# Optimization experiments

Hardware: AMD Instinct MI355X
Metric: run time of the kernel (lower is better)

## Reference

```python
import jax, jax.numpy as jnp
import numpy as np

N = 8192
D_IN = 128
D_OUT = 128

def setup_inputs() -> dict:
    key = jax.random.key(0)
    k_x, k_q, k_k, k_v = jax.random.split(key, 4)
    scale = 1.0 / np.sqrt(D_IN)
    return {
        "input": jax.random.normal(k_x, (N, D_IN), dtype=jnp.float32),
        # torch Linear weights: [out_features, in_features]
        "Wq": jax.random.normal(k_q, (D_IN, D_IN), dtype=jnp.float32) * scale,
        "Wk": jax.random.normal(k_k, (D_IN, D_IN), dtype=jnp.float32) * scale,
        "Wv": jax.random.normal(k_v, (D_OUT, D_IN), dtype=jnp.float32) * scale,
    }

def reference(input, Wq, Wk, Wv):
    # torch Linear: y = x @ W.T
    Q = input @ Wq.T          # [N, d_in]
    K = input @ Wk.T          # [N, d_in]
    V = input @ Wv.T          # [N, d_out]
    # NOTE: original module has NO 1/sqrt(d) scaling — keep it faithful.
    W = jax.nn.softmax(Q @ K.T, axis=-1)  # [N, N]
    return W @ V              # [N, d_out]
```

## Files before the change

kernel.cpp:

```cpp
#include <hip/hip_runtime.h>
#include <hip/hip_bf16.h>
#include <stdint.h>

#define N_TOK 8192
#define D 128
#define QTILES (N_TOK / 16)
#define KVB 64
#define KVTILES (N_TOK / KVB)

typedef __attribute__((ext_vector_type(8))) short short8;
typedef __attribute__((ext_vector_type(4))) short short4v;
typedef __attribute__((ext_vector_type(4))) float f32x4;
typedef __attribute__((ext_vector_type(8))) _Float16 half8;
typedef __attribute__((ext_vector_type(4))) _Float16 half4;
typedef __attribute__((ext_vector_type(2))) __fp16 fp16x2;

__device__ __forceinline__ ushort f2bf(float f) {
    union { float f; uint32_t u; } cv; cv.f = f;
    uint32_t u = cv.u;
    return (ushort)((u + 0x7fffu + ((u >> 16) & 1u)) >> 16);
}
__device__ __forceinline__ float bf2f(ushort h) {
    union { uint32_t u; float f; } cv; cv.u = ((uint32_t)h) << 16;
    return cv.f;
}
__device__ __forceinline__ f32x4 zero4() {
    f32x4 z; z[0] = 0.f; z[1] = 0.f; z[2] = 0.f; z[3] = 0.f; return z;
}

__global__ void cvt_kernel(const float* __restrict__ Wq, const float* __restrict__ Wk,
                           const float* __restrict__ Wv,
                           ushort* __restrict__ Whi, ushort* __restrict__ Wlo) {
    int i = blockIdx.x * blockDim.x + threadIdx.x;
    int w = i * 4;
    if (w >= 3 * 16384) return;
    int m = w >> 14;
    int off = w & 16383;
    const float* src = (m == 0) ? Wq : ((m == 1) ? Wk : Wv);
    ushort* dhi = Whi + (m << 14);
    ushort* dlo = Wlo + (m << 14);
    f32x4 v = *(const f32x4*)(src + off);
    short4v ph, pl;
    #pragma unroll
    for (int r = 0; r < 4; ++r) {
        ushort h = f2bf(v[r]);
        ph[r] = (short)h;
        pl[r] = (short)f2bf(v[r] - bf2f(h));
    }
    *(short4v*)(dhi + off) = ph;
    *(short4v*)(dlo + off) = pl;
}

__global__ __launch_bounds__(256) void proj_kernel(
    const float* __restrict__ X,
    const ushort* __restrict__ Whi, const ushort* __restrict__ Wlo,
    ushort* __restrict__ Qh, ushort* __restrict__ Kh, ushort* __restrict__ Vt) {
    const int tid = threadIdx.x;
    const int lane = tid & 63;
    const int wid = tid >> 6;
    const int g = lane >> 4, r16 = lane & 15;
    const int nbase = blockIdx.x * 16;

    short8 xh[4], xl[4];
    const float* xr = X + (size_t)(nbase + r16) * D + 8 * g;
    #pragma unroll
    for (int ds = 0; ds < 4; ++ds) {
        f32x4 a = *(const f32x4*)(xr + 32 * ds);
        f32x4 b = *(const f32x4*)(xr + 32 * ds + 4);
        #pragma unroll
        for (int j = 0; j < 4; ++j) {
            ushort h = f2bf(a[j]);
            xh[ds][j] = (short)h;
            xl[ds][j] = (short)f2bf(a[j] - bf2f(h));
            ushort h2 = f2bf(b[j]);
            xh[ds][4 + j] = (short)h2;
            xl[ds][4 + j] = (short)f2bf(b[j] - bf2f(h2));
        }
    }

    #pragma unroll
    for (int m = 0; m < 2; ++m) {
        const ushort* Wh = Whi + m * 16384;
        const ushort* Wl = Wlo + m * 16384;
        ushort* O = m ? Kh : Qh;
        #pragma unroll
        for (int jj = 0; jj < 2; ++jj) {
            int jt = 2 * wid + jj;
            f32x4 acc = zero4();
            const ushort* wrh = Wh + (size_t)(16 * jt + r16) * D + 8 * g;
            const ushort* wrl = Wl + (size_t)(16 * jt + r16) * D + 8 * g;
            #pragma unroll
            for (int ds = 0; ds < 4; ++ds) {
                short8 wh = *(const short8*)(wrh + 32 * ds);
                short8 wl = *(const short8*)(wrl + 32 * ds);
                acc = __builtin_amdgcn_mfma_f32_16x16x32_bf16(wh, xh[ds], acc, 0, 0, 0);
                acc = __builtin_amdgcn_mfma_f32_16x16x32_bf16(wh, xl[ds], acc, 0, 0, 0);
                acc = __builtin_amdgcn_mfma_f32_16x16x32_bf16(wl, xh[ds], acc, 0, 0, 0);
            }
            half4 pk;
            #pragma unroll
            for (int r = 0; r < 4; ++r) pk[r] = (_Float16)acc[r];
            *(half4*)(O + (size_t)(nbase + r16) * D + 16 * jt + 4 * g) = pk;
        }
    }
    {
        const ushort* Wh = Whi + 32768;
        const ushort* Wl = Wlo + 32768;
        #pragma unroll
        for (int jj = 0; jj < 2; ++jj) {
            int jt = 2 * wid + jj;
            f32x4 acc = zero4();
            const ushort* wrh = Wh + (size_t)(16 * jt + r16) * D + 8 * g;
            const ushort* wrl = Wl + (size_t)(16 * jt + r16) * D + 8 * g;
            #pragma unroll
            for (int ds = 0; ds < 4; ++ds) {
                short8 wh = *(const short8*)(wrh + 32 * ds);
                short8 wl = *(const short8*)(wrl + 32 * ds);
                acc = __builtin_amdgcn_mfma_f32_16x16x32_bf16(xh[ds], wh, acc, 0, 0, 0);
                acc = __builtin_amdgcn_mfma_f32_16x16x32_bf16(xl[ds], wh, acc, 0, 0, 0);
                acc = __builtin_amdgcn_mfma_f32_16x16x32_bf16(xh[ds], wl, acc, 0, 0, 0);
            }
            half4 pk;
            #pragma unroll
            for (int r = 0; r < 4; ++r) pk[r] = (_Float16)acc[r];
            *(half4*)(Vt + (size_t)(16 * jt + r16) * N_TOK + nbase + 4 * g) = pk;
        }
    }
}

template<int NS>
__global__ __launch_bounds__(256, 2) void flash_kernel(
    const ushort* __restrict__ Qh, const ushort* __restrict__ Kh,
    const ushort* __restrict__ Vt, ushort* __restrict__ Opb, float* __restrict__ ML) {
    __shared__ __align__(16) ushort K_lds[2][KVB * D];
    __shared__ __align__(16) ushort V_lds[2][D * KVB];
    __shared__ __align__(16) ushort P_lds[4 * 2048];

    const int tid = threadIdx.x;
    const int lane = tid & 63;
    const int wid = tid >> 6;
    const int g = lane >> 4, r16 = lane & 15;
    const int sp = blockIdx.x % NS;
    const int qg = blockIdx.x / NS;
    const int t0 = (KVTILES * sp) / NS;
    const int t1 = (KVTILES * (sp + 1)) / NS;
    const int qbase = qg * 128 + wid * 32;
    const int pswz = (r16 & 7) << 3;

    half8 qf[2][4];
    #pragma unroll
    for (int qa = 0; qa < 2; ++qa) {
        const ushort* qr = Qh + (size_t)(qbase + 16 * qa + r16) * D + 8 * g;
        #pragma unroll
        for (int ds = 0; ds < 4; ++ds)
            qf[qa][ds] = *(const half8*)(qr + 32 * ds);
    }

    float m[2] = {-INFINITY, -INFINITY}, l[2] = {0.f, 0.f};
    f32x4 o[2][8];
    #pragma unroll
    for (int qa = 0; qa < 2; ++qa)
        #pragma unroll
        for (int dt = 0; dt < 8; ++dt) o[qa][dt] = zero4();

    ushort* P_w = &P_lds[wid * 2048];

    short8 sk[4], sv[4];

    auto LOADT = [&](int it) {
        const int kv = it * KVB;
        #pragma unroll
        for (int rr = 0; rr < 4; ++rr) {
            int idx = tid + 256 * rr;
            int row = idx >> 4, seg = idx & 15;
            sk[rr] = *(const short8*)(Kh + (size_t)(kv + row) * D + seg * 8);
        }
        #pragma unroll
        for (int rr = 0; rr < 4; ++rr) {
            int idx = tid + 256 * rr;
            int row = idx >> 3, seg = idx & 7;
            sv[rr] = *(const short8*)(Vt + (size_t)row * N_TOK + kv + seg * 8);
        }
    };
    auto WRITET = [&](int b) {
        #pragma unroll
        for (int rr = 0; rr < 4; ++rr) {
            int idx = tid + 256 * rr;
            int row = idx >> 4, seg = idx & 15;
            *(short8*)&K_lds[b][(row * 128 + seg * 8) ^ ((row & 7) << 3)] = sk[rr];
        }
        #pragma unroll
        for (int rr = 0; rr < 4; ++rr) {
            int idx = tid + 256 * rr;
            int row = idx >> 3, seg = idx & 7;
            *(short8*)&V_lds[b][(row * 64 + seg * 8) ^ ((row & 7) << 3)] = sv[rr];
        }
    };

    LOADT(t0);
    WRITET(0);
    __syncthreads();

    int buf = 0;
    for (int it = t0; it < t1; ++it) {
        if (it + 1 < t1) LOADT(it + 1);

        const ushort* kb = K_lds[buf];
        const ushort* vb = V_lds[buf];

        f32x4 s[2][4];
        #pragma unroll
        for (int qa = 0; qa < 2; ++qa)
            #pragma unroll
            for (int t = 0; t < 4; ++t) s[qa][t] = zero4();
        __builtin_amdgcn_s_setprio(1);
        #pragma unroll
        for (int t = 0; t < 4; ++t) {
            #pragma unroll
            for (int ds = 0; ds < 4; ++ds) {
                int row = 16 * t + r16;
                half8 kf = *(const half8*)&kb[(row * 128 + 32 * ds + 8 * g) ^ ((row & 7) << 3)];
                #pragma unroll
                for (int qa = 0; qa < 2; ++qa)
                    s[qa][t] = __builtin_amdgcn_mfma_f32_16x16x32_f16(kf, qf[qa][ds], s[qa][t], 0, 0, 0);
            }
        }
        __builtin_amdgcn_s_setprio(0);

        #pragma unroll
        for (int qa = 0; qa < 2; ++qa) {
            float tm = -INFINITY;
            #pragma unroll
            for (int t = 0; t < 4; ++t)
                #pragma unroll
                for (int r = 0; r < 4; ++r) tm = fmaxf(tm, s[qa][t][r]);
            tm = fmaxf(tm, __shfl_xor(tm, 16));
            tm = fmaxf(tm, __shfl_xor(tm, 32));
            if (!__all(tm <= m[qa])) {
                float mnew = fmaxf(m[qa], tm);
                float scale = __expf(m[qa] - mnew);
                l[qa] *= scale;
                #pragma unroll
                for (int dt = 0; dt < 8; ++dt) o[qa][dt] *= scale;
                m[qa] = mnew;
            }
            float psum = 0.f;
            #pragma unroll
            for (int t = 0; t < 4; ++t) {
                float p0 = __expf(s[qa][t][0] - m[qa]);
                float p1 = __expf(s[qa][t][1] - m[qa]);
                float p2 = __expf(s[qa][t][2] - m[qa]);
                float p3 = __expf(s[qa][t][3] - m[qa]);
                psum += (p0 + p1) + (p2 + p3);
                union { fp16x2 h[2]; short4v s4; } u;
                u.h[0] = __builtin_amdgcn_cvt_pkrtz(p0, p1);
                u.h[1] = __builtin_amdgcn_cvt_pkrtz(p2, p3);
                *(short4v*)&P_w[(qa * 1024 + r16 * 64 + 16 * t + 4 * g) ^ pswz] = u.s4;
            }
            psum += __shfl_xor(psum, 16);
            psum += __shfl_xor(psum, 32);
            l[qa] += psum;
        }

        __builtin_amdgcn_s_setprio(1);
        #pragma unroll
        for (int c = 0; c < 2; ++c) {
            half8 pf0 = *(const half8*)&P_w[(r16 * 64 + 32 * c + 8 * g) ^ pswz];
            half8 pf1 = *(const half8*)&P_w[(1024 + r16 * 64 + 32 * c + 8 * g) ^ pswz];
            #pragma unroll
            for (int dt = 0; dt < 8; ++dt) {
                int row = 16 * dt + r16;
                half8 vf = *(const half8*)&vb[(row * 64 + 32 * c + 8 * g) ^ ((row & 7) << 3)];
                o[0][dt] = __builtin_amdgcn_mfma_f32_16x16x32_f16(vf, pf0, o[0][dt], 0, 0, 0);
                o[1][dt] = __builtin_amdgcn_mfma_f32_16x16x32_f16(vf, pf1, o[1][dt], 0, 0, 0);
            }
        }
        __builtin_amdgcn_s_setprio(0);

        if (it + 1 < t1) WRITET(buf ^ 1);
        __syncthreads();
        buf ^= 1;
    }

    #pragma unroll
    for (int qa = 0; qa < 2; ++qa) {
        ushort* obase = Opb + ((size_t)sp * N_TOK + qbase + 16 * qa + r16) * D + 4 * g;
        #pragma unroll
        for (int dt = 0; dt < 8; ++dt) {
            half4 pk;
            #pragma unroll
            for (int r = 0; r < 4; ++r) pk[r] = (_Float16)o[qa][dt][r];
            *(half4*)(obase + 16 * dt) = pk;
        }
        if (g == 0) {
            int qt = (qbase + 16 * qa) >> 4;
            float* ml = ML + ((size_t)sp * QTILES + qt) * 32;
            ml[r16] = m[qa];
            ml[16 + r16] = l[qa];
        }
    }
}

template<int NS>
__global__ void merge_kernel(const ushort* __restrict__ Opb, const float* __restrict__ ML,
                             float* __restrict__ out) {
    int i = blockIdx.x * blockDim.x + threadIdx.x;
    int e = i * 4;
    if (e >= N_TOK * D) return;
    int q = e >> 7;
    int qt = q >> 4, qr = q & 15;
    float mv[NS], lv[NS];
    float M = -INFINITY;
    #pragma unroll
    for (int s = 0; s < NS; ++s) {
        const float* ml = ML + ((size_t)s * QTILES + qt) * 32;
        mv[s] = ml[qr];
        lv[s] = ml[16 + qr];
        M = fmaxf(M, mv[s]);
    }
    float L = 0.f, a[NS];
    #pragma unroll
    for (int s = 0; s < NS; ++s) { a[s] = __expf(mv[s] - M); L += a[s] * lv[s]; }
    float inv = 1.f / L;
    f32x4 acc = zero4();
    #pragma unroll
    for (int s = 0; s < NS; ++s) {
        half4 ov = *(const half4*)(Opb + (size_t)s * N_TOK * D + e);
        #pragma unroll
        for (int r = 0; r < 4; ++r) acc[r] += (float)ov[r] * a[s];
    }
    *(f32x4*)(out + e) = acc * inv;
}

extern "C" void kernel_launch(void* const* d_in, const int* in_sizes, int n_in,
                              void* d_out, int out_size, void* d_ws, size_t ws_size,
                              hipStream_t stream) {
    const float* X  = (const float*)d_in[0];
    const float* Wq = (const float*)d_in[1];
    const float* Wk = (const float*)d_in[2];
    const float* Wv = (const float*)d_in[3];
    float* out = (float*)d_out;

    char* ws = (char*)d_ws;
    ushort* Whi = (ushort*)(ws);
    ushort* Wlo = (ushort*)(ws + 98304);
    ushort* Qh  = (ushort*)(ws + 196608);
    ushort* Kh  = (ushort*)(ws + 2293760);
    ushort* Vt  = (ushort*)(ws + 4390912);
    ushort* Opb = (ushort*)(ws + 6488064);

    const size_t op_off = 6488064;
    const size_t need8 = op_off + (size_t)8 * N_TOK * D * 2 + (size_t)8 * QTILES * 32 * 4;

    cvt_kernel<<<48, 256, 0, stream>>>(Wq, Wk, Wv, Whi, Wlo);
    proj_kernel<<<QTILES, 256, 0, stream>>>(X, Whi, Wlo, Qh, Kh, Vt);

    if (ws_size >= need8) {
        float* ML = (float*)(ws + op_off + (size_t)8 * N_TOK * D * 2);
        flash_kernel<8><<<(N_TOK / 128) * 8, 256, 0, stream>>>(Qh, Kh, Vt, Opb, ML);
        merge_kernel<8><<<(N_TOK * D / 4 + 255) / 256, 256, 0, stream>>>(Opb, ML, out);
    } else {
        float* ML = (float*)(ws + op_off + (size_t)4 * N_TOK * D * 2);
        flash_kernel<4><<<(N_TOK / 128) * 4, 256, 0, stream>>>(Qh, Kh, Vt, Opb, ML);
        merge_kernel<4><<<(N_TOK * D / 4 + 255) / 256, 256, 0, stream>>>(Opb, ML, out);
    }
}
```

Before: 81.40 us.

## Fold log2e into Q projection, use exp2, and retile projection kernel

Q is multiplied by log2(e) before it is stored as fp16, so the flash and merge kernels can call exp2f directly instead of __expf, which saves a multiply per exponential. The projection kernel is retiled so each wave computes all 128 output columns for 32 tokens, instead of a 16-token block split across waves. This reuses weight fragments across two query subtiles but launches only 64 blocks, which may underfill the GPU. The row max is also computed as a balanced tree to shorten the dependency chain.

```diff
diff --git a/kernel.cpp b/kernel.cpp
--- a/kernel.cpp
+++ b/kernel.cpp
@@ -7,6 +7,7 @@
 #define QTILES (N_TOK / 16)
 #define KVB 64
 #define KVTILES (N_TOK / KVB)
+#define LOG2E 1.4426950408889634f
 
 typedef __attribute__((ext_vector_type(8))) short short8;
 typedef __attribute__((ext_vector_type(4))) short short4v;
@@ -26,6 +27,14 @@
 }
 __device__ __forceinline__ f32x4 zero4() {
     f32x4 z; z[0] = 0.f; z[1] = 0.f; z[2] = 0.f; z[3] = 0.f; return z;
+}
+__device__ __forceinline__ float max16(const f32x4* s) {
+    float a = fmaxf(fmaxf(s[0][0], s[0][1]), s[0][2]);
+    float b = fmaxf(fmaxf(s[0][3], s[1][0]), s[1][1]);
+    float c = fmaxf(fmaxf(s[1][2], s[1][3]), s[2][0]);
+    float d = fmaxf(fmaxf(s[2][1], s[2][2]), s[2][3]);
+    float e = fmaxf(fmaxf(s[3][0], s[3][1]), s[3][2]);
+    return fmaxf(fmaxf(fmaxf(a, b), c), fmaxf(fmaxf(d, e), s[3][3]));
 }
 
 __global__ void cvt_kernel(const float* __restrict__ Wq, const float* __restrict__ Wk,
@@ -59,22 +68,25 @@
     const int lane = tid & 63;
     const int wid = tid >> 6;
     const int g = lane >> 4, r16 = lane & 15;
-    const int nbase = blockIdx.x * 16;
-
-    short8 xh[4], xl[4];
-    const float* xr = X + (size_t)(nbase + r16) * D + 8 * g;
-    #pragma unroll
-    for (int ds = 0; ds < 4; ++ds) {
-        f32x4 a = *(const f32x4*)(xr + 32 * ds);
-        f32x4 b = *(const f32x4*)(xr + 32 * ds + 4);
-        #pragma unroll
-        for (int j = 0; j < 4; ++j) {
-            ushort h = f2bf(a[j]);
-            xh[ds][j] = (short)h;
-            xl[ds][j] = (short)f2bf(a[j] - bf2f(h));
-            ushort h2 = f2bf(b[j]);
-            xh[ds][4 + j] = (short)h2;
-            xl[ds][4 + j] = (short)f2bf(b[j] - bf2f(h2));
+    const int qbase = blockIdx.x * 128 + wid * 32;
+
+    short8 xh[2][4], xl[2][4];
+    #pragma unroll
+    for (int qa = 0; qa < 2; ++qa) {
+        const float* xr = X + (size_t)(qbase + 16 * qa + r16) * D + 8 * g;
+        #pragma unroll
+        for (int ds = 0; ds < 4; ++ds) {
+            f32x4 a = *(const f32x4*)(xr + 32 * ds);
+            f32x4 b = *(const f32x4*)(xr + 32 * ds + 4);
+            #pragma unroll
+            for (int j = 0; j < 4; ++j) {
+                ushort h = f2bf(a[j]);
+                xh[qa][ds][j] = (short)h;
+                xl[qa][ds][j] = (short)f2bf(a[j] - bf2f(h));
+                ushort h2 = f2bf(b[j]);
+                xh[qa][ds][4 + j] = (short)h2;
+                xl[qa][ds][4 + j] = (short)f2bf(b[j] - bf2f(h2));
+            }
         }
     }
 
@@ -83,47 +95,58 @@
         const ushort* Wh = Whi + m * 16384;
         const ushort* Wl = Wlo + m * 16384;
         ushort* O = m ? Kh : Qh;
-        #pragma unroll
-        for (int jj = 0; jj < 2; ++jj) {
-            int jt = 2 * wid + jj;
-            f32x4 acc = zero4();
+        const float sc = m ? 1.0f : LOG2E;
+        #pragma unroll
+        for (int jt = 0; jt < 8; ++jt) {
             const ushort* wrh = Wh + (size_t)(16 * jt + r16) * D + 8 * g;
             const ushort* wrl = Wl + (size_t)(16 * jt + r16) * D + 8 * g;
+            f32x4 acc[2] = {zero4(), zero4()};
             #pragma unroll
             for (int ds = 0; ds < 4; ++ds) {
                 short8 wh = *(const short8*)(wrh + 32 * ds);
                 short8 wl = *(const short8*)(wrl + 32 * ds);
-                acc = __builtin_amdgcn_mfma_f32_16x16x32_bf16(wh, xh[ds], acc, 0, 0, 0);
-                acc = __builtin_amdgcn_mfma_f32_16x16x32_bf16(wh, xl[ds], acc, 0, 0, 0);
-                acc = __builtin_amdgcn_mfma_f32_16x16x32_bf16(wl, xh[ds], acc, 0, 0, 0);
-            }
-            half4 pk;
-            #pragma unroll
-            for (int r = 0; r < 4; ++r) pk[r] = (_Float16)acc[r];
-            *(half4*)(O + (size_t)(nbase + r16) * D + 16 * jt + 4 * g) = pk;
+                #pragma unroll
+                for (int qa = 0; qa < 2; ++qa) {
+                    acc[qa] = __builtin_amdgcn_mfma_f32_16x16x32_bf16(wh, xh[qa][ds], acc[qa], 0, 0, 0);
+                    acc[qa] = __builtin_amdgcn_mfma_f32_16x16x32_bf16(wh, xl[qa][ds], acc[qa], 0, 0, 0);
+                    acc[qa] = __builtin_amdgcn_mfma_f32_16x16x32_bf16(wl, xh[qa][ds], acc[qa], 0, 0, 0);
+                }
+            }
+            #pragma unroll
+            for (int qa = 0; qa < 2; ++qa) {
+                half4 pk;
+                #pragma unroll
+                for (int r = 0; r < 4; ++r) pk[r] = (_Float16)(acc[qa][r] * sc);
+                *(half4*)(O + (size_t)(qbase + 16 * qa + r16) * D + 16 * jt + 4 * g) = pk;
+            }
         }
     }
     {
         const ushort* Wh = Whi + 32768;
         const ushort* Wl = Wlo + 32768;
         #pragma unroll
-        for (int jj = 0; jj < 2; ++jj) {
-            int jt = 2 * wid + jj;
-            f32x4 acc = zero4();
+        for (int jt = 0; jt < 8; ++jt) {
             const ushort* wrh = Wh + (size_t)(16 * jt + r16) * D + 8 * g;
             const ushort* wrl = Wl + (size_t)(16 * jt + r16) * D + 8 * g;
+            f32x4 acc[2] = {zero4(), zero4()};
             #pragma unroll
             for (int ds = 0; ds < 4; ++ds) {
                 short8 wh = *(const short8*)(wrh + 32 * ds);
                 short8 wl = *(const short8*)(wrl + 32 * ds);
-                acc = __builtin_amdgcn_mfma_f32_16x16x32_bf16(xh[ds], wh, acc, 0, 0, 0);
-                acc = __builtin_amdgcn_mfma_f32_16x16x32_bf16(xl[ds], wh, acc, 0, 0, 0);
-                acc = __builtin_amdgcn_mfma_f32_16x16x32_bf16(xh[ds], wl, acc, 0, 0, 0);
-            }
-            half4 pk;
-            #pragma unroll
-            for (int r = 0; r < 4; ++r) pk[r] = (_Float16)acc[r];
-            *(half4*)(Vt + (size_t)(16 * jt + r16) * N_TOK + nbase + 4 * g) = pk;
+                #pragma unroll
+                for (int qa = 0; qa < 2; ++qa) {
+                    acc[qa] = __builtin_amdgcn_mfma_f32_16x16x32_bf16(xh[qa][ds], wh, acc[qa], 0, 0, 0);
+                    acc[qa] = __builtin_amdgcn_mfma_f32_16x16x32_bf16(xl[qa][ds], wh, acc[qa], 0, 0, 0);
+                    acc[qa] = __builtin_amdgcn_mfma_f32_16x16x32_bf16(xh[qa][ds], wl, acc[qa], 0, 0, 0);
+                }
+            }
+            #pragma unroll
+            for (int qa = 0; qa < 2; ++qa) {
+                half4 pk;
+                #pragma unroll
+                for (int r = 0; r < 4; ++r) pk[r] = (_Float16)acc[qa][r];
+                *(half4*)(Vt + (size_t)(16 * jt + r16) * N_TOK + qbase + 16 * qa + 4 * g) = pk;
+            }
         }
     }
 }
@@ -229,16 +252,12 @@
 
         #pragma unroll
         for (int qa = 0; qa < 2; ++qa) {
-            float tm = -INFINITY;
-            #pragma unroll
-            for (int t = 0; t < 4; ++t)
-                #pragma unroll
-                for (int r = 0; r < 4; ++r) tm = fmaxf(tm, s[qa][t][r]);
+            float tm = max16(s[qa]);
             tm = fmaxf(tm, __shfl_xor(tm, 16));
             tm = fmaxf(tm, __shfl_xor(tm, 32));
             if (!__all(tm <= m[qa])) {
                 float mnew = fmaxf(m[qa], tm);
-                float scale = __expf(m[qa] - mnew);
+                float scale = exp2f(m[qa] - mnew);
                 l[qa] *= scale;
                 #pragma unroll
                 for (int dt = 0; dt < 8; ++dt) o[qa][dt] *= scale;
@@ -247,10 +266,10 @@
             float psum = 0.f;
             #pragma unroll
             for (int t = 0; t < 4; ++t) {
-                float p0 = __expf(s[qa][t][0] - m[qa]);
-                float p1 = __expf(s[qa][t][1] - m[qa]);
-                float p2 = __expf(s[qa][t][2] - m[qa]);
-                float p3 = __expf(s[qa][t][3] - m[qa]);
+                float p0 = exp2f(s[qa][t][0] - m[qa]);
+                float p1 = exp2f(s[qa][t][1] - m[qa]);
+                float p2 = exp2f(s[qa][t][2] - m[qa]);
+                float p3 = exp2f(s[qa][t][3] - m[qa]);
                 psum += (p0 + p1) + (p2 + p3);
                 union { fp16x2 h[2]; short4v s4; } u;
                 u.h[0] = __builtin_amdgcn_cvt_pkrtz(p0, p1);
@@ -320,7 +339,7 @@
     }
     float L = 0.f, a[NS];
     #pragma unroll
-    for (int s = 0; s < NS; ++s) { a[s] = __expf(mv[s] - M); L += a[s] * lv[s]; }
+    for (int s = 0; s < NS; ++s) { a[s] = exp2f(mv[s] - M); L += a[s] * lv[s]; }
     float inv = 1.f / L;
     f32x4 acc = zero4();
     #pragma unroll
@@ -353,7 +372,7 @@
     const size_t need8 = op_off + (size_t)8 * N_TOK * D * 2 + (size_t)8 * QTILES * 32 * 4;
 
     cvt_kernel<<<48, 256, 0, stream>>>(Wq, Wk, Wv, Whi, Wlo);
-    proj_kernel<<<QTILES, 256, 0, stream>>>(X, Whi, Wlo, Qh, Kh, Vt);
+    proj_kernel<<<64, 256, 0, stream>>>(X, Whi, Wlo, Qh, Kh, Vt);
 
     if (ws_size >= need8) {
         float* ML = (float*)(ws + op_off + (size_t)8 * N_TOK * D * 2);
```

Measured after the change: 103.6 us. +27.3%, slower.
